# Kernel optimization log

Measured on AMD Instinct MI355X. Metric: run time of the kernel, lower is better.

The kernel has to match this reference:

```python
import jax, jax.numpy as jnp
import numpy as np

ALPHA = 0.2  # LeakyReLU slope
BN_EPS = 1e-5


def _conv_circ(x, w, b, pad_w):
    # circular padding only on width (torch padding=(0, pad_w), padding_mode='circular')
    x = jnp.pad(x, ((0, 0), (0, 0), (0, 0), (pad_w, pad_w)), mode='wrap')
    y = jax.lax.conv_general_dilated(x, w, window_strides=(1, 1), padding='VALID',
                                     dimension_numbers=('NCHW', 'OIHW', 'NCHW'))
    return y + b[None, :, None, None]


def _graph_conv(x, n, w, b, pad_w):
    h1 = _conv_circ(x, w, b, pad_w)  # [B, N, C, F]
    h2 = _conv_circ(n, w, b, pad_w)
    B, N, C, F = h1.shape
    h1f = h1.reshape(B, N, C * F)
    h2f = h2.reshape(B, N, C * F)
    a = jnp.einsum('bnf,bmf->bnm', h1f, h2f)          # [B, N, N]
    a = jnp.where(a > 0, a, ALPHA * a)                 # LeakyReLU
    att = jax.nn.softmax(a, axis=1)                    # torch Softmax(dim=1)
    return (att @ h1f).reshape(B, N, C, F)


def _bn_pool_relu(x, gamma, beta, mean, var):
    # eval-mode BatchNorm2d -> MaxPool2d((1,2)) -> ReLU
    inv = gamma / jnp.sqrt(var + BN_EPS)
    x = x * inv[None, :, None, None] + (beta - mean * inv)[None, :, None, None]
    W = x.shape[-1]
    W2 = (W // 2) * 2
    x = x[..., :W2].reshape(*x.shape[:-1], W2 // 2, 2).max(axis=-1)
    return jax.nn.relu(x)


def setup_inputs() -> dict:
    key = jax.random.key(0)
    ks = jax.random.split(key, 16)
    B = 16384
    return {
        'x': jax.random.normal(ks[0], (B, 5, 5, 50), jnp.float32),
        'conv1_w': jax.random.normal(ks[1], (32, 5, 5, 11), jnp.float32) * 0.1,
        'conv1_b': jax.random.normal(ks[2], (32,), jnp.float32) * 0.1,
        'bn1_gamma': jax.random.uniform(ks[3], (32,), jnp.float32, 0.5, 1.5),
        'bn1_beta': jax.random.normal(ks[4], (32,), jnp.float32) * 0.1,
        'bn1_mean': jax.random.normal(ks[5], (32,), jnp.float32) * 0.1,
        'bn1_var': jax.random.uniform(ks[6], (32,), jnp.float32, 0.5, 1.5),
        'conv2_w': jax.random.normal(ks[7], (32, 32, 1, 5), jnp.float32) * 0.1,
        'conv2_b': jax.random.normal(ks[8], (32,), jnp.float32) * 0.1,
        'bn2_gamma': jax.random.uniform(ks[9], (32,), jnp.float32, 0.5, 1.5),
        'bn2_beta': jax.random.normal(ks[10], (32,), jnp.float32) * 0.1,
        'bn2_mean': jax.random.normal(ks[11], (32,), jnp.float32) * 0.1,
        'bn2_var': jax.random.uniform(ks[12], (32,), jnp.float32, 0.5, 1.5),
        'lin_w': jax.random.normal(ks[13], (13, 384), jnp.float32) * 0.05,
        'lin_b': jax.random.normal(ks[14], (13,), jnp.float32) * 0.05,
    }


def reference(x, conv1_w, conv1_b, bn1_gamma, bn1_beta, bn1_mean, bn1_var,
              conv2_w, conv2_b, bn2_gamma, bn2_beta, bn2_mean, bn2_var,
              lin_w, lin_b):
    W = x.shape[-1]
    xa, na = x[..., :W // 2], x[..., W // 2:]
    xa = _graph_conv(xa, xa, conv1_w, conv1_b, 5)
    na = _graph_conv(na, na, conv1_w, conv1_b, 5)
    xa = _bn_pool_relu(xa, bn1_gamma, bn1_beta, bn1_mean, bn1_var)
    na = _bn_pool_relu(na, bn1_gamma, bn1_beta, bn1_mean, bn1_var)
    x2 = _graph_conv(xa, na, conv2_w, conv2_b, 2)
    n2 = _graph_conv(na, xa, conv2_w, conv2_b, 2)
    x2 = _bn_pool_relu(x2, bn2_gamma, bn2_beta, bn2_mean, bn2_var)
    n2 = _bn_pool_relu(n2, bn2_gamma, bn2_beta, bn2_mean, bn2_var)
    flat = jnp.concatenate([x2, n2], axis=-1).reshape(x.shape[0], -1)  # [B, 384]
    # Dropout(0.2) is identity in eval mode
    return flat @ lin_w.T + lin_b
```

## Files before the change

### kernel.cpp

```cpp
#include <hip/hip_runtime.h>
#include <math.h>

#define ALPHA 0.2f
#define BN_EPS 1e-5f

typedef __attribute__((ext_vector_type(8))) short short8;
typedef __attribute__((ext_vector_type(4))) float v4f;

__device__ __forceinline__ unsigned short f2bf_rne(float f) {
    union { float f; unsigned u; } x; x.f = f;
    unsigned r = x.u + 0x7FFFu + ((x.u >> 16) & 1u);
    return (unsigned short)(r >> 16);
}
__device__ __forceinline__ float bf2f(unsigned short h) {
    union { float f; unsigned u; } x; x.u = ((unsigned)h) << 16;
    return x.f;
}
__device__ __forceinline__ unsigned cvtpk_bf16(float a0, float a1) {
    unsigned r;
    asm("v_cvt_pk_bf16_f32 %0, %1, %2" : "=v"(r) : "v"(a0), "v"(a1));
    return r;
}
__device__ __forceinline__ void hilo_pair(float a0, float a1, unsigned& hp, unsigned& lp) {
    hp = cvtpk_bf16(a0, a1);
    union { unsigned u; float f; } c0, c1;
    c0.u = hp << 16; c1.u = hp & 0xFFFF0000u;
    lp = cvtpk_bf16(a0 - c0.f, a1 - c1.f);
}
__device__ __forceinline__ unsigned funnel16(unsigned hi, unsigned lo, int sh) {
    return (unsigned)((((unsigned long long)hi << 32) | lo) >> sh);
}

__global__ __launch_bounds__(256) void prep_kernel(const float* __restrict__ w1,
                                                   const float* __restrict__ w2,
                                                   unsigned short* __restrict__ ws16) {
    int s = blockIdx.x * 256 + threadIdx.x;
    if (s < 1664) {
        int lane = s & 63;
        int ktnt = s >> 6;
        int Kt = ktnt % 13;
        int Nt = ktnt / 13;
        int oc = Nt * 16 + (lane & 15);
        int quad = lane >> 4;
        for (int j = 0; j < 8; ++j) {
            int kp = Kt * 32 + quad * 8 + j;
            int kw = kp & 15, ickh = kp >> 4;
            float w = 0.f;
            if (kw < 11 && ickh < 25) w = w1[oc * 275 + ickh * 11 + kw];
            unsigned short h = f2bf_rne(w);
            ws16[s * 8 + j] = h;
            ws16[13312 + s * 8 + j] = f2bf_rne(w - bf2f(h));
        }
    } else if (s < 2304) {
        int s2 = s - 1664;
        int lane = s2 & 63;
        int ktnt = s2 >> 6;
        int kw = ktnt >> 1;
        int nt = ktnt & 1;
        int oc = nt * 16 + (lane & 15);
        int quad = lane >> 4;
        for (int j = 0; j < 8; ++j) {
            int ic = quad * 8 + j;
            float w = w2[oc * 160 + ic * 5 + kw];
            unsigned short h = f2bf_rne(w);
            ws16[26624 + s2 * 8 + j] = h;
            ws16[31744 + s2 * 8 + j] = f2bf_rne(w - bf2f(h));
        }
    }
}

#define IT 2984
#define HLO 858
#define XB 1716
#define CSTO 5968
#define LDS_TOTAL (5968 + 128)

__global__ __launch_bounds__(256, 6) void gcn_kernel(
    const float* __restrict__ x,
    const float* __restrict__ w1, const float* __restrict__ b1,
    const float* __restrict__ g1, const float* __restrict__ be1,
    const float* __restrict__ mu1, const float* __restrict__ va1,
    const float* __restrict__ w2, const float* __restrict__ b2,
    const float* __restrict__ g2, const float* __restrict__ be2,
    const float* __restrict__ mu2, const float* __restrict__ va2,
    const float* __restrict__ lw, const float* __restrict__ lb,
    const unsigned short* __restrict__ ws16,
    float* __restrict__ out)
{
    __shared__ float lds[LDS_TOTAL];
    float* cst = lds + CSTO;

    const int tid = threadIdx.x;
    const int b0  = blockIdx.x * 2;

    {
        const float2* xg2 = (const float2*)(x + (size_t)b0 * 1250);
        for (int i2 = tid; i2 < 1250; i2 += 256) {
            float2 v = xg2[i2];
            int i = 2 * i2;
            int it = (i >= 1250) ? 1 : 0;
            int j = i - it * 1250;
            unsigned short* XU = (unsigned short*)(lds + it * IT + XB);
            {
                int c = j / 250; int r = j - c * 250;
                int h = r / 50;  int w50 = r - h * 50;
                int ha = (w50 >= 25) ? 1 : 0;
                int w = w50 - ha * 25;
                int base = (ha * 25 + c * 5 + h) * 42;
                unsigned short u = f2bf_rne(v.x);
                XU[base + 5 + w] = u;
                if (w >= 20) XU[base + w - 20] = u;
                if (w <= 9)  XU[base + 30 + w] = u;
            }
            {
                int j1 = j + 1;
                int c = j1 / 250; int r = j1 - c * 250;
                int h = r / 50;  int w51 = r - h * 50;
                int hb = (w51 >= 25) ? 1 : 0;
                int w = w51 - hb * 25;
                int base = (hb * 25 + c * 5 + h) * 42;
                unsigned short u = f2bf_rne(v.y);
                XU[base + 5 + w] = u;
                if (w >= 20) XU[base + w - 20] = u;
                if (w <= 9)  XU[base + 30 + w] = u;
            }
        }
        if (tid < 42) {
            int itz = (tid >= 21) ? 1 : 0;
            lds[itz * IT + XB + 1050 + (tid - itz * 21)] = 0.f;
        }
    }
    if (tid < 64) {
        int oc = tid & 31;
        if (tid < 32) {
            float inv = g1[oc] * rsqrtf(va1[oc] + BN_EPS);
            cst[oc]      = inv;
            cst[32 + oc] = be1[oc] - mu1[oc] * inv;
        } else {
            float inv = g2[oc] * rsqrtf(va2[oc] + BN_EPS);
            cst[64 + oc] = inv;
            cst[96 + oc] = be2[oc] - mu2[oc] * inv;
        }
    }
    __syncthreads();

    {
        const int wave = tid >> 6, lane = tid & 63;
        const int it = wave >> 1;
        const int Mtb = (wave & 1) * 2;
        const int quad = lane >> 4, m16 = lane & 15;
        const int kw0 = (quad & 1) * 8;
        const int ickh0 = quad >> 1;
        const unsigned* XD = (const unsigned*)(lds + it * IT + XB);

        int ub[2], sh[2];
#pragma unroll
        for (int mt = 0; mt < 2; ++mt) {
            int mg = (Mtb + mt) * 16 + m16;
            int half = mg >> 5, pos = mg & 31;
            int ux = (half * 25 + ickh0) * 42 + pos + kw0;
            ub[mt] = ux >> 1;
            sh[mt] = (ux & 1) << 4;
        }

        v4f zz = {0.f, 0.f, 0.f, 0.f};
        v4f acc[2][2];
        acc[0][0] = zz; acc[0][1] = zz; acc[1][0] = zz; acc[1][1] = zz;

        for (int Kt = 0; Kt < 13; ++Kt) {
            union { unsigned u[4]; short8 v; } af[2];
#pragma unroll
            for (int mt = 0; mt < 2; ++mt) {
                int b = ub[mt] + Kt * 42;
                unsigned d0 = XD[b + 0], d1 = XD[b + 1], d2 = XD[b + 2];
                unsigned d3 = XD[b + 3], d4 = XD[b + 4];
                af[mt].u[0] = funnel16(d1, d0, sh[mt]);
                af[mt].u[1] = funnel16(d2, d1, sh[mt]);
                af[mt].u[2] = funnel16(d3, d2, sh[mt]);
                af[mt].u[3] = funnel16(d4, d3, sh[mt]);
            }
#pragma unroll
            for (int nt = 0; nt < 2; ++nt) {
                const short8* ph = (const short8*)(ws16 + ((nt * 13 + Kt) * 64 + lane) * 8);
                const short8* pl = (const short8*)(ws16 + 13312 + ((nt * 13 + Kt) * 64 + lane) * 8);
                short8 bh = *ph;
                short8 bl = *pl;
#pragma unroll
                for (int mt = 0; mt < 2; ++mt) {
                    acc[mt][nt] = __builtin_amdgcn_mfma_f32_16x16x32_bf16(af[mt].v, bh, acc[mt][nt], 0, 0, 0);
                    acc[mt][nt] = __builtin_amdgcn_mfma_f32_16x16x32_bf16(af[mt].v, bl, acc[mt][nt], 0, 0, 0);
                }
            }
        }

        float biasv0 = b1[m16], biasv1 = b1[16 + m16];
        unsigned* HD = (unsigned*)(lds + it * IT);
#pragma unroll
        for (int mt = 0; mt < 2; ++mt) {
#pragma unroll
            for (int rr = 0; rr < 2; ++rr) {
                int mg0 = (Mtb + mt) * 16 + quad * 4 + rr * 2;
                int half = mg0 >> 5, pos0 = mg0 & 31;
                if (pos0 <= 24) {
                    int kd = pos0 >> 1;
#pragma unroll
                    for (int nt = 0; nt < 2; ++nt) {
                        float bias = nt ? biasv1 : biasv0;
                        float v0 = acc[mt][nt][rr * 2] + bias;
                        float v1 = acc[mt][nt][rr * 2 + 1] + bias;
                        unsigned hp, lp;
                        hilo_pair(v0, v1, hp, lp);
                        int ch = half * 32 + nt * 16 + m16;
                        HD[kd * 66 + ch] = hp;
                        HD[858 + kd * 66 + ch] = lp;
                    }
                }
            }
        }
    }
    __syncthreads();

    {
        const int wave = tid >> 6, lane = tid & 63;
        const int it = wave >> 1, half = wave & 1;
        const int m16 = lane & 15, q = lane >> 4;
        const unsigned* D = (const unsigned*)(lds + it * IT);
        short8 fh[2], fl[2];
#pragma unroll
        for (int t = 0; t < 2; ++t) {
            int row = half * 32 + t * 16 + m16;
            union { unsigned u[4]; short8 v; } H, L;
#pragma unroll
            for (int i = 0; i < 4; ++i) {
                int k0 = q * 8 + 2 * i;
                unsigned mh = D[(k0 >> 1) * 66 + row];
                unsigned ml = D[858 + (k0 >> 1) * 66 + row];
                if (k0 == 24) { mh &= 0xFFFFu; ml &= 0xFFFFu; }
                if (k0 > 24)  { mh = 0u; ml = 0u; }
                H.u[i] = mh; L.u[i] = ml;
            }
            fh[t] = H.v; fl[t] = L.v;
        }
        v4f zz = {0.f, 0.f, 0.f, 0.f};
        v4f acc[2][2];
        acc[0][0] = zz; acc[0][1] = zz; acc[1][0] = zz; acc[1][1] = zz;
#pragma unroll
        for (int mt = 0; mt < 2; ++mt)
#pragma unroll
            for (int nt = 0; nt < 2; ++nt) {
                acc[mt][nt] = __builtin_amdgcn_mfma_f32_16x16x32_bf16(fh[mt], fh[nt], acc[mt][nt], 0, 0, 0);
                acc[mt][nt] = __builtin_amdgcn_mfma_f32_16x16x32_bf16(fh[mt], fl[nt], acc[mt][nt], 0, 0, 0);
                acc[mt][nt] = __builtin_amdgcn_mfma_f32_16x16x32_bf16(fl[mt], fh[nt], acc[mt][nt], 0, 0, 0);
            }
        __syncthreads();
        float* A = &lds[it * IT + HLO];
#pragma unroll
        for (int mt = 0; mt < 2; ++mt)
#pragma unroll
            for (int nt = 0; nt < 2; ++nt)
#pragma unroll
                for (int r = 0; r < 4; ++r) {
                    int m = mt * 16 + q * 4 + r;
                    int n = nt * 16 + m16;
                    float s = acc[mt][nt][r];
                    s = (s > 0.f) ? s : ALPHA * s;
                    A[(half * 32 + m) * 33 + n] = s;
                }
    }
    __syncthreads();

    {
        int row = tid >> 1, q = tid & 1;
        int it = row >> 6, rm = row & 63;
        float* rp = &lds[it * IT + HLO + rm * 33];
        float ev[16];
        float mx = -INFINITY;
#pragma unroll
        for (int k = 0; k < 16; ++k) { ev[k] = rp[q + 2 * k]; mx = fmaxf(mx, ev[k]); }
        mx = fmaxf(mx, __shfl_xor(mx, 1));
        float s = 0.f;
#pragma unroll
        for (int k = 0; k < 16; ++k) { ev[k] = __expf(ev[k] - mx); s += ev[k]; }
        s += __shfl_xor(s, 1);
        float inv = 1.f / s;
#pragma unroll
        for (int k = 0; k < 16; ++k) rp[q + 2 * k] = ev[k] * inv;
    }
    __syncthreads();

    {
        const int wave = tid >> 6, lane = tid & 63;
        const int it = wave >> 1, half = wave & 1;
        const int m16 = lane & 15, q = lane >> 4;
        const unsigned short* U = (const unsigned short*)(lds + it * IT);
        const float* AT = &lds[it * IT + HLO];

        short8 ah[2];
#pragma unroll
        for (int mt = 0; mt < 2; ++mt) {
            int pos = mt * 16 + m16;
            int kd = pos >> 1, par = pos & 1;
            union { unsigned u[4]; short8 v; } H;
#pragma unroll
            for (int i = 0; i < 4; ++i) {
                int ch = half * 32 + q * 8 + 2 * i;
                unsigned h0 = U[kd * 132 + ch * 2 + par];
                unsigned h1u = U[kd * 132 + (ch + 1) * 2 + par];
                H.u[i] = h0 | (h1u << 16);
            }
            ah[mt] = H.v;
        }
        short8 bh[2], bl[2];
#pragma unroll
        for (int nt = 0; nt < 2; ++nt) {
            union { unsigned u[4]; short8 v; } H, L;
#pragma unroll
            for (int i = 0; i < 4; ++i) {
                int m = q * 8 + 2 * i;
                float a0 = AT[(half * 32 + m) * 33 + nt * 16 + m16];
                float a1 = AT[(half * 32 + m + 1) * 33 + nt * 16 + m16];
                unsigned hp, lp;
                hilo_pair(a0, a1, hp, lp);
                H.u[i] = hp; L.u[i] = lp;
            }
            bh[nt] = H.v; bl[nt] = L.v;
        }
        v4f zz = {0.f, 0.f, 0.f, 0.f};
        v4f acc[2][2];
        acc[0][0] = zz; acc[0][1] = zz; acc[1][0] = zz; acc[1][1] = zz;
#pragma unroll
        for (int mt = 0; mt < 2; ++mt)
#pragma unroll
            for (int nt = 0; nt < 2; ++nt) {
                acc[mt][nt] = __builtin_amdgcn_mfma_f32_16x16x32_bf16(ah[mt], bh[nt], acc[mt][nt], 0, 0, 0);
                acc[mt][nt] = __builtin_amdgcn_mfma_f32_16x16x32_bf16(ah[mt], bl[nt], acc[mt][nt], 0, 0, 0);
            }

        __syncthreads();

        unsigned short* PT = (unsigned short*)(lds + it * IT) + half * 832;
#pragma unroll
        for (int mt = 0; mt < 2; ++mt)
#pragma unroll
            for (int nt = 0; nt < 2; ++nt) {
                int n = nt * 16 + m16;
                float inv = cst[n], sh = cst[32 + n];
#pragma unroll
                for (int rr = 0; rr < 2; ++rr) {
                    int pos0 = mt * 16 + q * 4 + rr * 2;
                    if (pos0 < 24) {
                        float v0 = acc[mt][nt][rr * 2] * inv + sh;
                        float v1 = acc[mt][nt][rr * 2 + 1] * inv + sh;
                        float p = fmaxf(fmaxf(v0, v1), 0.f);
                        int j = pos0 >> 1;
                        unsigned short h = f2bf_rne(p);
                        PT[(n >> 1) * 26 + j * 2 + (n & 1)] = h;
                        PT[416 + (n >> 1) * 26 + j * 2 + (n & 1)] = f2bf_rne(p - bf2f(h));
                    }
                }
            }
    }
    __syncthreads();

    {
        const int wave = tid >> 6, lane = tid & 63;
        const int it = wave >> 1, half = wave & 1;
        const int m16 = lane & 15, q = lane >> 4;
        const unsigned* PTD = (const unsigned*)(lds + it * IT) + half * 416;

        v4f zz = {0.f, 0.f, 0.f, 0.f};
        v4f acc[2]; acc[0] = zz; acc[1] = zz;
#pragma unroll
        for (int kw = 0; kw < 5; ++kw) {
            int owr = m16 + kw - 2;
            if (owr < 0) owr += 12;
            if (owr >= 12) owr -= 12;
            union { unsigned u[4]; short8 v; } H, L;
#pragma unroll
            for (int i = 0; i < 4; ++i) {
                H.u[i] = PTD[(q * 4 + i) * 13 + owr];
                L.u[i] = PTD[208 + (q * 4 + i) * 13 + owr];
            }
#pragma unroll
            for (int nt = 0; nt < 2; ++nt) {
                const short8* ph = (const short8*)(ws16 + 26624 + ((kw * 2 + nt) * 64 + lane) * 8);
                const short8* pl = (const short8*)(ws16 + 31744 + ((kw * 2 + nt) * 64 + lane) * 8);
                short8 wbh = *ph, wbl = *pl;
                acc[nt] = __builtin_amdgcn_mfma_f32_16x16x32_bf16(H.v, wbh, acc[nt], 0, 0, 0);
                acc[nt] = __builtin_amdgcn_mfma_f32_16x16x32_bf16(H.v, wbl, acc[nt], 0, 0, 0);
                acc[nt] = __builtin_amdgcn_mfma_f32_16x16x32_bf16(L.v, wbh, acc[nt], 0, 0, 0);
            }
        }

        __syncthreads();

        if (q < 3) {
            unsigned* H2 = (unsigned*)(lds + it * IT);
#pragma unroll
            for (int nt = 0; nt < 2; ++nt) {
                float bias = b2[nt * 16 + m16];
                int ch = half * 32 + nt * 16 + m16;
#pragma unroll
                for (int rr = 0; rr < 2; ++rr) {
                    float v0 = acc[nt][rr * 2] + bias;
                    float v1 = acc[nt][rr * 2 + 1] + bias;
                    unsigned hp, lp;
                    hilo_pair(v0, v1, hp, lp);
                    H2[(q * 2 + rr) * 66 + ch] = hp;
                    H2[396 + (q * 2 + rr) * 66 + ch] = lp;
                }
            }
        }
    }
    __syncthreads();

    {
        const int wave = tid >> 6, lane = tid & 63;
        const int it = wave >> 1, half = wave & 1;
        const int m16 = lane & 15, q = lane >> 4;
        const unsigned* D = (const unsigned*)(lds + it * IT);
        short8 ah[2], al[2], bh[2], bl[2];
#pragma unroll
        for (int t = 0; t < 2; ++t) {
            int rowA = (1 - half) * 32 + t * 16 + m16;
            int rowB = half * 32 + t * 16 + m16;
            union { unsigned u[4]; short8 v; } HA, LA, HB, LB;
#pragma unroll
            for (int i = 0; i < 4; ++i) {
                int k0 = q * 8 + 2 * i;
                unsigned a_h = D[(k0 >> 1) * 66 + rowA];
                unsigned a_l = D[396 + (k0 >> 1) * 66 + rowA];
                unsigned b_h = D[(k0 >> 1) * 66 + rowB];
                unsigned b_l = D[396 + (k0 >> 1) * 66 + rowB];
                if (k0 > 10) { a_h = 0u; a_l = 0u; b_h = 0u; b_l = 0u; }
                HA.u[i] = a_h; LA.u[i] = a_l; HB.u[i] = b_h; LB.u[i] = b_l;
            }
            ah[t] = HA.v; al[t] = LA.v; bh[t] = HB.v; bl[t] = LB.v;
        }
        v4f zz = {0.f, 0.f, 0.f, 0.f};
        v4f acc[2][2];
        acc[0][0] = zz; acc[0][1] = zz; acc[1][0] = zz; acc[1][1] = zz;
#pragma unroll
        for (int mt = 0; mt < 2; ++mt)
#pragma unroll
            for (int nt = 0; nt < 2; ++nt) {
                acc[mt][nt] = __builtin_amdgcn_mfma_f32_16x16x32_bf16(ah[mt], bh[nt], acc[mt][nt], 0, 0, 0);
                acc[mt][nt] = __builtin_amdgcn_mfma_f32_16x16x32_bf16(ah[mt], bl[nt], acc[mt][nt], 0, 0, 0);
                acc[mt][nt] = __builtin_amdgcn_mfma_f32_16x16x32_bf16(al[mt], bh[nt], acc[mt][nt], 0, 0, 0);
            }
        float* A = &lds[it * IT + HLO];
#pragma unroll
        for (int mt = 0; mt < 2; ++mt)
#pragma unroll
            for (int nt = 0; nt < 2; ++nt)
#pragma unroll
                for (int r = 0; r < 4; ++r) {
                    int m = mt * 16 + q * 4 + r;
                    int n = nt * 16 + m16;
                    float s = acc[mt][nt][r];
                    s = (s > 0.f) ? s : ALPHA * s;
                    A[(half * 32 + m) * 33 + n] = s;
                }
    }
    __syncthreads();

    {
        int row = tid >> 1, q = tid & 1;
        int it = row >> 6, rm = row & 63;
        float* rp = &lds[it * IT + HLO + rm * 33];
        float ev[16];
        float mx = -INFINITY;
#pragma unroll
        for (int k = 0; k < 16; ++k) { ev[k] = rp[q + 2 * k]; mx = fmaxf(mx, ev[k]); }
        mx = fmaxf(mx, __shfl_xor(mx, 1));
        float s = 0.f;
#pragma unroll
        for (int k = 0; k < 16; ++k) { ev[k] = __expf(ev[k] - mx); s += ev[k]; }
        s += __shfl_xor(s, 1);
        float inv = 1.f / s;
#pragma unroll
        for (int k = 0; k < 16; ++k) rp[q + 2 * k] = ev[k] * inv;
    }
    __syncthreads();

    {
        const int wave = tid >> 6, lane = tid & 63;
        const int it = wave >> 1, half = wave & 1;
        const int m16 = lane & 15, q = lane >> 4;
        const unsigned short* U = (const unsigned short*)(lds + it * IT);
        const float* AT = &lds[it * IT + HLO];

        int kd = m16 >> 1, par = m16 & 1;
        union { unsigned u[4]; short8 v; } HA, LA;
#pragma unroll
        for (int i = 0; i < 4; ++i) {
            int ch = half * 32 + q * 8 + 2 * i;
            unsigned h0 = U[kd * 132 + ch * 2 + par];
            unsigned h1u = U[kd * 132 + (ch + 1) * 2 + par];
            unsigned l0 = U[792 + kd * 132 + ch * 2 + par];
            unsigned l1 = U[792 + kd * 132 + (ch + 1) * 2 + par];
            HA.u[i] = h0 | (h1u << 16);
            LA.u[i] = l0 | (l1 << 16);
        }
        short8 bh[2], bl[2];
#pragma unroll
        for (int nt = 0; nt < 2; ++nt) {
            union { unsigned u[4]; short8 v; } H, L;
#pragma unroll
            for (int i = 0; i < 4; ++i) {
                int m = q * 8 + 2 * i;
                float a0 = AT[(half * 32 + m) * 33 + nt * 16 + m16];
                float a1 = AT[(half * 32 + m + 1) * 33 + nt * 16 + m16];
                unsigned hp, lp;
                hilo_pair(a0, a1, hp, lp);
                H.u[i] = hp; L.u[i] = lp;
            }
            bh[nt] = H.v; bl[nt] = L.v;
        }
        v4f zz = {0.f, 0.f, 0.f, 0.f};
        v4f acc[2]; acc[0] = zz; acc[1] = zz;
#pragma unroll
        for (int nt = 0; nt < 2; ++nt) {
            acc[nt] = __builtin_amdgcn_mfma_f32_16x16x32_bf16(HA.v, bh[nt], acc[nt], 0, 0, 0);
            acc[nt] = __builtin_amdgcn_mfma_f32_16x16x32_bf16(HA.v, bl[nt], acc[nt], 0, 0, 0);
            acc[nt] = __builtin_amdgcn_mfma_f32_16x16x32_bf16(LA.v, bh[nt], acc[nt], 0, 0, 0);
        }

        __syncthreads();

        if (q < 3) {
#pragma unroll
            for (int nt = 0; nt < 2; ++nt) {
                int n = nt * 16 + m16;
                float inv = cst[64 + n], sh = cst[96 + n];
#pragma unroll
                for (int rr = 0; rr < 2; ++rr) {
                    int j = q * 2 + rr;
                    float v0 = acc[nt][rr * 2] * inv + sh;
                    float v1 = acc[nt][rr * 2 + 1] * inv + sh;
                    lds[it * IT + n * 12 + half * 6 + j] =
                        fmaxf(fmaxf(v0, v1), 0.f);
                }
            }
        }
    }
    __syncthreads();

    if (tid < 208) {
        int s8 = tid & 7;
        int rest = tid >> 3;
        int it = (rest >= 13) ? 1 : 0;
        int o = rest - it * 13;
        const float4* wv4 = (const float4*)(lw + o * 384 + s8 * 48);
        const float4* fv4 = (const float4*)&lds[it * IT + s8 * 48];
        float s = 0.f;
#pragma unroll
        for (int i = 0; i < 12; ++i) {
            float4 w4 = wv4[i];
            float4 f4 = fv4[i];
            s += f4.x * w4.x + f4.y * w4.y + f4.z * w4.z + f4.w * w4.w;
        }
        s += __shfl_down(s, 4, 8);
        s += __shfl_down(s, 2, 8);
        s += __shfl_down(s, 1, 8);
        if (s8 == 0) out[(size_t)(b0 + it) * 13 + o] = s + lb[o];
    }
}

extern "C" void kernel_launch(void* const* d_in, const int* in_sizes, int n_in,
                              void* d_out, int out_size, void* d_ws, size_t ws_size,
                              hipStream_t stream) {
    const float* x   = (const float*)d_in[0];
    const float* w1  = (const float*)d_in[1];
    const float* b1  = (const float*)d_in[2];
    const float* g1  = (const float*)d_in[3];
    const float* be1 = (const float*)d_in[4];
    const float* mu1 = (const float*)d_in[5];
    const float* va1 = (const float*)d_in[6];
    const float* w2  = (const float*)d_in[7];
    const float* b2  = (const float*)d_in[8];
    const float* g2  = (const float*)d_in[9];
    const float* be2 = (const float*)d_in[10];
    const float* mu2 = (const float*)d_in[11];
    const float* va2 = (const float*)d_in[12];
    const float* lw  = (const float*)d_in[13];
    const float* lb  = (const float*)d_in[14];
    float* out = (float*)d_out;
    unsigned short* ws16 = (unsigned short*)d_ws;

    prep_kernel<<<9, 256, 0, stream>>>(w1, w2, ws16);

    int B = in_sizes[0] / 1250;
    gcn_kernel<<<B / 2, 256, 0, stream>>>(x, w1, b1, g1, be1, mu1, va1,
                                          w2, b2, g2, be2, mu2, va2, lw, lb,
                                          ws16, out);
}
```

Measured before the change: 271.9 us.

## Reorder conv1 K dimension as kw-outer with channel-contiguous LDS layout

Restructures the first convolution's im2col: the input is staged in LDS transposed so the 25 (channel,row) values for each width position are contiguous, letting each MFMA A-fragment be a single aligned 16-byte LDS read instead of five dword reads plus funnel shifts. The K loop becomes 11 iterations over kernel width (32-wide K padded from 25) instead of 13 iterations of 32 over a kw-padded-to-16 layout, which cuts MFMA count and removes padding waste. The weight prep is reindexed to match. An extra __syncthreads is added before the LDS is overwritten with conv outputs, since the new input layout overlaps the output region.

```diff
diff --git a/kernel.cpp b/kernel.cpp
--- a/kernel.cpp
+++ b/kernel.cpp
@@ -27,32 +27,27 @@
     c0.u = hp << 16; c1.u = hp & 0xFFFF0000u;
     lp = cvtpk_bf16(a0 - c0.f, a1 - c1.f);
 }
-__device__ __forceinline__ unsigned funnel16(unsigned hi, unsigned lo, int sh) {
-    return (unsigned)((((unsigned long long)hi << 32) | lo) >> sh);
-}
 
 __global__ __launch_bounds__(256) void prep_kernel(const float* __restrict__ w1,
                                                    const float* __restrict__ w2,
                                                    unsigned short* __restrict__ ws16) {
     int s = blockIdx.x * 256 + threadIdx.x;
-    if (s < 1664) {
+    if (s < 1408) {
         int lane = s & 63;
         int ktnt = s >> 6;
-        int Kt = ktnt % 13;
-        int Nt = ktnt / 13;
-        int oc = Nt * 16 + (lane & 15);
+        int kw = ktnt >> 1;
+        int nt = ktnt & 1;
+        int oc = nt * 16 + (lane & 15);
         int quad = lane >> 4;
         for (int j = 0; j < 8; ++j) {
-            int kp = Kt * 32 + quad * 8 + j;
-            int kw = kp & 15, ickh = kp >> 4;
-            float w = 0.f;
-            if (kw < 11 && ickh < 25) w = w1[oc * 275 + ickh * 11 + kw];
+            int k = quad * 8 + j;
+            float w = (k < 25) ? w1[oc * 275 + k * 11 + kw] : 0.f;
             unsigned short h = f2bf_rne(w);
             ws16[s * 8 + j] = h;
-            ws16[13312 + s * 8 + j] = f2bf_rne(w - bf2f(h));
-        }
-    } else if (s < 2304) {
-        int s2 = s - 1664;
+            ws16[11264 + s * 8 + j] = f2bf_rne(w - bf2f(h));
+        }
+    } else if (s < 2048) {
+        int s2 = s - 1408;
         int lane = s2 & 63;
         int ktnt = s2 >> 6;
         int kw = ktnt >> 1;
@@ -63,15 +58,15 @@
             int ic = quad * 8 + j;
             float w = w2[oc * 160 + ic * 5 + kw];
             unsigned short h = f2bf_rne(w);
-            ws16[26624 + s2 * 8 + j] = h;
-            ws16[31744 + s2 * 8 + j] = f2bf_rne(w - bf2f(h));
+            ws16[22528 + s2 * 8 + j] = h;
+            ws16[27648 + s2 * 8 + j] = f2bf_rne(w - bf2f(h));
         }
     }
 }
 
 #define IT 2984
 #define HLO 858
-#define XB 1716
+#define XKT 860
 #define CSTO 5968
 #define LDS_TOTAL (5968 + 128)
 
@@ -87,48 +82,56 @@
     const unsigned short* __restrict__ ws16,
     float* __restrict__ out)
 {
-    __shared__ float lds[LDS_TOTAL];
+    __shared__ __align__(16) float lds[LDS_TOTAL];
     float* cst = lds + CSTO;
 
     const int tid = threadIdx.x;
     const int b0  = blockIdx.x * 2;
 
-    {
-        const float2* xg2 = (const float2*)(x + (size_t)b0 * 1250);
-        for (int i2 = tid; i2 < 1250; i2 += 256) {
-            float2 v = xg2[i2];
-            int i = 2 * i2;
-            int it = (i >= 1250) ? 1 : 0;
-            int j = i - it * 1250;
-            unsigned short* XU = (unsigned short*)(lds + it * IT + XB);
+    if (tid < 250) {
+        int rowid = tid / 5;
+        int s = tid - rowid * 5;
+        int it = (rowid >= 25) ? 1 : 0;
+        int k = rowid - it * 25;
+        const float2* src = (const float2*)(x + (size_t)b0 * 1250) + it * 625 + k * 25 + s * 5;
+        unsigned short* XU = (unsigned short*)(lds + it * IT + XKT);
+#pragma unroll
+        for (int e = 0; e < 5; ++e) {
+            float2 v = src[e];
+            int w50 = s * 10 + 2 * e;
             {
-                int c = j / 250; int r = j - c * 250;
-                int h = r / 50;  int w50 = r - h * 50;
-                int ha = (w50 >= 25) ? 1 : 0;
-                int w = w50 - ha * 25;
-                int base = (ha * 25 + c * 5 + h) * 42;
+                int half = (w50 >= 25) ? 1 : 0;
+                int w = w50 - half * 25;
                 unsigned short u = f2bf_rne(v.x);
-                XU[base + 5 + w] = u;
-                if (w >= 20) XU[base + w - 20] = u;
-                if (w <= 9)  XU[base + 30 + w] = u;
+                int a = half * 1400 + (w + 5) * 40 + k;
+                XU[a] = u;
+                if (w >= 20) XU[a - 1000] = u;
+                if (w <= 4)  XU[a + 1000] = u;
             }
             {
-                int j1 = j + 1;
-                int c = j1 / 250; int r = j1 - c * 250;
-                int h = r / 50;  int w51 = r - h * 50;
-                int hb = (w51 >= 25) ? 1 : 0;
-                int w = w51 - hb * 25;
-                int base = (hb * 25 + c * 5 + h) * 42;
+                int w51 = w50 + 1;
+                int half = (w51 >= 25) ? 1 : 0;
+                int w = w51 - half * 25;
                 unsigned short u = f2bf_rne(v.y);
-                XU[base + 5 + w] = u;
-                if (w >= 20) XU[base + w - 20] = u;
-                if (w <= 9)  XU[base + 30 + w] = u;
-            }
-        }
-        if (tid < 42) {
-            int itz = (tid >= 21) ? 1 : 0;
-            lds[itz * IT + XB + 1050 + (tid - itz * 21)] = 0.f;
-        }
+                int a = half * 1400 + (w + 5) * 40 + k;
+                XU[a] = u;
+                if (w >= 20) XU[a - 1000] = u;
+                if (w <= 4)  XU[a + 1000] = u;
+            }
+        }
+    }
+    if (tid < 140) {
+        int it = (tid >= 70) ? 1 : 0;
+        int r2 = tid - it * 70;
+        int half = (r2 >= 35) ? 1 : 0;
+        int w3 = r2 - half * 35;
+        int a = half * 1400 + w3 * 40;
+        unsigned short* XU = (unsigned short*)(lds + it * IT + XKT);
+        XU[a + 25] = 0;
+        unsigned* XD = (unsigned*)XU;
+        XD[(a >> 1) + 13] = 0;
+        XD[(a >> 1) + 14] = 0;
+        XD[(a >> 1) + 15] = 0;
     }
     if (tid < 64) {
         int oc = tid & 31;
@@ -149,49 +152,38 @@
         const int it = wave >> 1;
         const int Mtb = (wave & 1) * 2;
         const int quad = lane >> 4, m16 = lane & 15;
-        const int kw0 = (quad & 1) * 8;
-        const int ickh0 = quad >> 1;
-        const unsigned* XD = (const unsigned*)(lds + it * IT + XB);
-
-        int ub[2], sh[2];
+        const unsigned* XK = (const unsigned*)(lds + it * IT + XKT);
+
+        int ab[2];
 #pragma unroll
         for (int mt = 0; mt < 2; ++mt) {
             int mg = (Mtb + mt) * 16 + m16;
             int half = mg >> 5, pos = mg & 31;
-            int ux = (half * 25 + ickh0) * 42 + pos + kw0;
-            ub[mt] = ux >> 1;
-            sh[mt] = (ux & 1) << 4;
+            pos = (pos > 24) ? 24 : pos;
+            ab[mt] = half * 700 + pos * 20 + quad * 4;
         }
 
         v4f zz = {0.f, 0.f, 0.f, 0.f};
         v4f acc[2][2];
         acc[0][0] = zz; acc[0][1] = zz; acc[1][0] = zz; acc[1][1] = zz;
 
-        for (int Kt = 0; Kt < 13; ++Kt) {
-            union { unsigned u[4]; short8 v; } af[2];
-#pragma unroll
-            for (int mt = 0; mt < 2; ++mt) {
-                int b = ub[mt] + Kt * 42;
-                unsigned d0 = XD[b + 0], d1 = XD[b + 1], d2 = XD[b + 2];
-                unsigned d3 = XD[b + 3], d4 = XD[b + 4];
-                af[mt].u[0] = funnel16(d1, d0, sh[mt]);
-                af[mt].u[1] = funnel16(d2, d1, sh[mt]);
-                af[mt].u[2] = funnel16(d3, d2, sh[mt]);
-                af[mt].u[3] = funnel16(d4, d3, sh[mt]);
-            }
-#pragma unroll
-            for (int nt = 0; nt < 2; ++nt) {
-                const short8* ph = (const short8*)(ws16 + ((nt * 13 + Kt) * 64 + lane) * 8);
-                const short8* pl = (const short8*)(ws16 + 13312 + ((nt * 13 + Kt) * 64 + lane) * 8);
+        for (int kw = 0; kw < 11; ++kw) {
+            short8 a0 = *(const short8*)(XK + ab[0] + kw * 20);
+            short8 a1 = *(const short8*)(XK + ab[1] + kw * 20);
+#pragma unroll
+            for (int nt = 0; nt < 2; ++nt) {
+                const short8* ph = (const short8*)(ws16 + ((kw * 2 + nt) * 64 + lane) * 8);
+                const short8* pl = (const short8*)(ws16 + 11264 + ((kw * 2 + nt) * 64 + lane) * 8);
                 short8 bh = *ph;
                 short8 bl = *pl;
-#pragma unroll
-                for (int mt = 0; mt < 2; ++mt) {
-                    acc[mt][nt] = __builtin_amdgcn_mfma_f32_16x16x32_bf16(af[mt].v, bh, acc[mt][nt], 0, 0, 0);
-                    acc[mt][nt] = __builtin_amdgcn_mfma_f32_16x16x32_bf16(af[mt].v, bl, acc[mt][nt], 0, 0, 0);
-                }
-            }
-        }
+                acc[0][nt] = __builtin_amdgcn_mfma_f32_16x16x32_bf16(a0, bh, acc[0][nt], 0, 0, 0);
+                acc[0][nt] = __builtin_amdgcn_mfma_f32_16x16x32_bf16(a0, bl, acc[0][nt], 0, 0, 0);
+                acc[1][nt] = __builtin_amdgcn_mfma_f32_16x16x32_bf16(a1, bh, acc[1][nt], 0, 0, 0);
+                acc[1][nt] = __builtin_amdgcn_mfma_f32_16x16x32_bf16(a1, bl, acc[1][nt], 0, 0, 0);
+            }
+        }
+
+        __syncthreads();
 
         float biasv0 = b1[m16], biasv1 = b1[16 + m16];
         unsigned* HD = (unsigned*)(lds + it * IT);
@@ -383,8 +375,8 @@
             }
 #pragma unroll
             for (int nt = 0; nt < 2; ++nt) {
-                const short8* ph = (const short8*)(ws16 + 26624 + ((kw * 2 + nt) * 64 + lane) * 8);
-                const short8* pl = (const short8*)(ws16 + 31744 + ((kw * 2 + nt) * 64 + lane) * 8);
+                const short8* ph = (const short8*)(ws16 + 22528 + ((kw * 2 + nt) * 64 + lane) * 8);
+                const short8* pl = (const short8*)(ws16 + 27648 + ((kw * 2 + nt) * 64 + lane) * 8);
                 short8 wbh = *ph, wbl = *pl;
                 acc[nt] = __builtin_amdgcn_mfma_f32_16x16x32_bf16(H.v, wbh, acc[nt], 0, 0, 0);
                 acc[nt] = __builtin_amdgcn_mfma_f32_16x16x32_bf16(H.v, wbl, acc[nt], 0, 0, 0);
@@ -588,7 +580,7 @@
     float* out = (float*)d_out;
     unsigned short* ws16 = (unsigned short*)d_ws;
 
-    prep_kernel<<<9, 256, 0, stream>>>(w1, w2, ws16);
+    prep_kernel<<<8, 256, 0, stream>>>(w1, w2, ws16);
 
     int B = in_sizes[0] / 1250;
     gcn_kernel<<<B / 2, 256, 0, stream>>>(x, w1, b1, g1, be1, mu1, va1,
```

Measured after the change: 245.6 us. -9.7%, faster.
